# Kernel optimization log

Measured on AMD Instinct MI355X. Metric: run time of the kernel, lower is better.

The kernel has to match this reference:

```python
import jax, jax.numpy as jnp
import numpy as np

NUM_NODES = 17
NUM_REL = 8  # 4 edge types, doubled with reverse edges
IN_DIM = HID_DIM = OUT_DIM = 2048


def _build_graph():
    # Hardcoded brain graph from _build_brain_graph()
    # signals 0-5, emotions 6-11, cognitions 12-16
    src = np.array([0,0,1,1,2,2,3,3,4,4,5,5,          # signal->emotion (type 0)
                    6,6,7,7,8,8,8,9,9,10,11,11,       # emotion->cognition (type 1)
                    6,9,7,10,8,11,6,8,7,8,            # emotion<->emotion (type 2)
                    0,1,2])                            # signal->cognition (type 3)
    dst = np.array([7,10,6,9,9,7,10,7,6,9,9,6,
                    15,12,14,13,12,13,16,16,12,14,16,12,
                    9,6,10,7,11,8,8,6,8,7,
                    12,12,13])
    typ = np.array([0]*12 + [1]*12 + [2]*10 + [3]*3)
    # edge_index = cat([E, E.flip(0)]); edge_type = cat([t, t + 4])
    ei = np.stack([np.concatenate([src, dst]), np.concatenate([dst, src])])
    et = np.concatenate([typ, typ + 4])
    return jnp.asarray(ei, jnp.int32), jnp.asarray(et, jnp.int32)


def setup_inputs() -> dict:
    key = jax.random.key(0)
    ks = jax.random.split(key, 6)
    s = 0.02  # init scale
    edge_index, edge_type = _build_graph()
    return {
        'node_emb': jax.random.normal(ks[0], (NUM_NODES, IN_DIM), jnp.float32),
        'signal_features': jax.random.normal(ks[1], (6, IN_DIM), jnp.float32),
        'W1': jax.random.normal(ks[2], (NUM_REL, IN_DIM, HID_DIM), jnp.float32) * s,
        'root1': jax.random.normal(ks[3], (IN_DIM, HID_DIM), jnp.float32) * s,
        'bias1': jnp.zeros((HID_DIM,), jnp.float32),
        'W2': jax.random.normal(ks[4], (NUM_REL, HID_DIM, OUT_DIM), jnp.float32) * s,
        'root2': jax.random.normal(ks[5], (HID_DIM, OUT_DIM), jnp.float32) * s,
        'bias2': jnp.zeros((OUT_DIM,), jnp.float32),
        'edge_index': edge_index,
        'edge_type': edge_type,
    }


def _rgcn(x, W, root, bias, src, dst, etype):
    """PyG-style RGCNConv: per-relation linear + per-relation mean aggregation + root + bias."""
    # Transform all 17 nodes by all relations at once: [R, N, H] (tiny activation, avoids
    # gathering a [E, d, h] weight tensor per edge).
    xW = jnp.einsum('nd,rdh->rnh', x, W)
    msg = xW[etype, src]                                  # [E, H]
    seg = etype * NUM_NODES + dst                         # segment per (relation, target)
    sums = jax.ops.segment_sum(msg, seg, num_segments=NUM_REL * NUM_NODES)
    cnt = jax.ops.segment_sum(jnp.ones((msg.shape[0],), x.dtype), seg,
                              num_segments=NUM_REL * NUM_NODES)
    mean = sums / jnp.maximum(cnt, 1.0)[:, None]          # per-relation mean aggr
    agg = mean.reshape(NUM_REL, NUM_NODES, -1).sum(0)     # sum over relations
    return agg + x @ root + bias


def reference(node_emb, signal_features, W1, root1, bias1, W2, root2, bias2,
              edge_index, edge_type):
    src, dst = edge_index[0], edge_index[1]
    # h = node_emb(arange(17)); h[:6] = signal_features
    h = node_emb.at[:signal_features.shape[0]].set(signal_features)
    h1 = jax.nn.relu(_rgcn(h, W1, root1, bias1, src, dst, edge_type))
    # dropout is identity in eval mode
    h2 = _rgcn(h1, W2, root2, bias2, src, dst, edge_type)
    return h2
```

## Files before the change

kernel.cpp:

```cpp
#include <hip/hip_runtime.h>
#include <hip/hip_bf16.h>

#define D 2048
#define NTASK 55
#define NAGG 38
#define CHUNK 64
#define NCH 32

__constant__ int c_grp[10] = {0, 4, 9, 15, 17, 23, 29, 35, 38, 55};

__constant__ int c_src[74] = {
    1,4,5,  0,2,3,  1,2,4,5,  0,3,
    6,8,9,11,  7,8,  7,10,  6,  8,9,11,
    9,8,  10,8,  11,6,7,  6,  7,  8,
    0,1,  2,
    7,10,  6,9,  9,7,  10,7,  6,9,  9,6,
    15,12,  14,13,  12,13,16,  16,12,  14,  16,12,
    9,8,  10,8,  11,6,7,  6,  7,  8,
    12, 12, 13
};
__constant__ int c_off[39] = {
    0,3,6,10,12, 16,18,20,21,24, 26,28,31,32,33, 34,36,
    37,39,41,43,45,47, 49,51,53,56,58,59, 61,63,65,68,69,70, 71,72,73,74
};

__constant__ int c_node_tasks[38] = {
    17,35,  18,36,  19,37,  20,  21,  22,
    0,9,23,29,  1,10,24,30,  11,25,31,  2,12,26,32,  3,13,27,33,  14,28,34,
    4,15,  5,16,  6,  7,  8
};
__constant__ int c_node_off[18] = {0,2,4,6,7,8,9,13,17,20,24,28,31,33,35,36,37,38};

__global__ __launch_bounds__(256) void prep_kernel(
        const float* __restrict__ emb, const float* __restrict__ sig,
        float* __restrict__ U, float* __restrict__ TO) {
    int t = blockIdx.x;
    int tid = threadIdx.x;
    if (t >= NAGG) {
        int v = t - NAGG;
        const float* h = (v < 6) ? sig + (size_t)v * D : emb + (size_t)v * D;
        for (int c = tid; c < D; c += 256) {
            U[(size_t)t * D + c] = h[c];
            TO[(size_t)t * D + c] = 0.f;
        }
    } else {
        int o0 = c_off[t], o1 = c_off[t + 1];
        float cnt = (float)(o1 - o0);
        for (int c = tid; c < D; c += 256) {
            float s = 0.f;
            for (int o = o0; o < o1; ++o) {
                int sn = c_src[o];
                const float* h = (sn < 6) ? sig + (size_t)sn * D : emb + (size_t)sn * D;
                s += h[c];
            }
            U[(size_t)t * D + c] = s / cnt;
            TO[(size_t)t * D + c] = 0.f;
        }
    }
}

template <int NG>
__device__ __forceinline__ void gemm_inner(
        const float* __restrict__ Wg, const float* su,
        float* __restrict__ TO, int tb, int d0, int col) {
    float4 acc[NG];
#pragma unroll
    for (int t = 0; t < NG; ++t) acc[t] = make_float4(0.f, 0.f, 0.f, 0.f);
#pragma unroll 4
    for (int dd = 0; dd < CHUNK; ++dd) {
        float4 w = *reinterpret_cast<const float4*>(Wg + (size_t)(d0 + dd) * D + col);
#pragma unroll
        for (int t = 0; t < NG; ++t) {
            float u = su[t * CHUNK + dd];
            acc[t].x = fmaf(u, w.x, acc[t].x);
            acc[t].y = fmaf(u, w.y, acc[t].y);
            acc[t].z = fmaf(u, w.z, acc[t].z);
            acc[t].w = fmaf(u, w.w, acc[t].w);
        }
    }
#pragma unroll
    for (int t = 0; t < NG; ++t) {
        float* p = TO + (size_t)(tb + t) * D + col;
        atomicAdd(p + 0, acc[t].x);
        atomicAdd(p + 1, acc[t].y);
        atomicAdd(p + 2, acc[t].z);
        atomicAdd(p + 3, acc[t].w);
    }
}

__global__ __launch_bounds__(256) void gemm_kernel(
        const float* __restrict__ U, const float* __restrict__ W,
        const float* __restrict__ root, float* __restrict__ TO) {
    int b = blockIdx.x;
    int g = b >> 6;
    int r = b & 63;
    int ct = r & 1;
    int ch = r >> 1;
    int d0 = ch * CHUNK;
    int col = ct * 1024 + threadIdx.x * 4;
    const float* Wg = (g < 8) ? W + (size_t)g * D * D : root;
    int tb = c_grp[g];
    int ng = c_grp[g + 1] - tb;

    __shared__ float su[17 * CHUNK];
    for (int i = threadIdx.x; i < ng * CHUNK; i += 256) {
        int t = i >> 6, dd = i & (CHUNK - 1);
        su[i] = U[(size_t)(tb + t) * D + d0 + dd];
    }
    __syncthreads();

    switch (ng) {
        case 2:  gemm_inner<2>(Wg, su, TO, tb, d0, col); break;
        case 3:  gemm_inner<3>(Wg, su, TO, tb, d0, col); break;
        case 4:  gemm_inner<4>(Wg, su, TO, tb, d0, col); break;
        case 5:  gemm_inner<5>(Wg, su, TO, tb, d0, col); break;
        case 6:  gemm_inner<6>(Wg, su, TO, tb, d0, col); break;
        default: gemm_inner<17>(Wg, su, TO, tb, d0, col); break;
    }
}

__global__ __launch_bounds__(256) void mid_kernel(
        const float* __restrict__ bias, float* __restrict__ U,
        float* __restrict__ TO) {
    int c = blockIdx.x * 256 + threadIdx.x;
    int tid = threadIdx.x;
    __shared__ float h1s[17 * 256];
#pragma unroll
    for (int v = 0; v < 17; ++v) {
        float s = bias[c] + TO[(size_t)(NAGG + v) * D + c];
        for (int o = c_node_off[v]; o < c_node_off[v + 1]; ++o)
            s += TO[(size_t)c_node_tasks[o] * D + c];
        s = fmaxf(s, 0.f);
        h1s[v * 256 + tid] = s;
    }
    for (int t = 0; t < NAGG; ++t) {
        int o0 = c_off[t], o1 = c_off[t + 1];
        float s = 0.f;
        for (int o = o0; o < o1; ++o) s += h1s[c_src[o] * 256 + tid];
        U[(size_t)t * D + c] = s / (float)(o1 - o0);
        TO[(size_t)t * D + c] = 0.f;
    }
#pragma unroll
    for (int v = 0; v < 17; ++v) {
        U[(size_t)(NAGG + v) * D + c] = h1s[v * 256 + tid];
        TO[(size_t)(NAGG + v) * D + c] = 0.f;
    }
}

__global__ __launch_bounds__(256) void final_kernel(
        const float* __restrict__ TO, const float* __restrict__ bias,
        float* __restrict__ out) {
    int c = blockIdx.x * 256 + threadIdx.x;
#pragma unroll
    for (int v = 0; v < 17; ++v) {
        float s = bias[c] + TO[(size_t)(NAGG + v) * D + c];
        for (int o = c_node_off[v]; o < c_node_off[v + 1]; ++o)
            s += TO[(size_t)c_node_tasks[o] * D + c];
        out[(size_t)v * D + c] = s;
    }
}

extern "C" void kernel_launch(void* const* d_in, const int* in_sizes, int n_in,
                              void* d_out, int out_size, void* d_ws, size_t ws_size,
                              hipStream_t stream) {
    const float* emb   = (const float*)d_in[0];
    const float* sig   = (const float*)d_in[1];
    const float* W1    = (const float*)d_in[2];
    const float* root1 = (const float*)d_in[3];
    const float* b1    = (const float*)d_in[4];
    const float* W2    = (const float*)d_in[5];
    const float* root2 = (const float*)d_in[6];
    const float* b2    = (const float*)d_in[7];
    float* out = (float*)d_out;

    float* U  = (float*)d_ws;
    float* TO = U + (size_t)NTASK * D;

    prep_kernel<<<NTASK, 256, 0, stream>>>(emb, sig, U, TO);
    gemm_kernel<<<9 * 2 * NCH, 256, 0, stream>>>(U, W1, root1, TO);
    mid_kernel<<<D / 256, 256, 0, stream>>>(b1, U, TO);
    gemm_kernel<<<9 * 2 * NCH, 256, 0, stream>>>(U, W2, root2, TO);
    final_kernel<<<D / 256, 256, 0, stream>>>(TO, b2, out);
}
```

Before: 449.5 us.

## Replace atomic split-K accumulation with partial buffers and double-buffered weight loads

The GEMM no longer reduces split-K chunks with float atomicAdds into a zeroed accumulator. Each chunk writes its partials to its own slice of a P buffer, and the reduction over 32 chunks moves into the mid and final kernels, which now run across more blocks. Weight loads in the GEMM inner loop are software-pipelined with two 8-row register buffers so memory latency overlaps the FMAs. This removes atomic contention and the zeroing writes, but adds extra partial-buffer traffic, more register pressure, and one more kernel launch.

```diff
diff --git a/kernel.cpp b/kernel.cpp
--- a/kernel.cpp
+++ b/kernel.cpp
@@ -33,19 +33,17 @@
 
 __global__ __launch_bounds__(256) void prep_kernel(
         const float* __restrict__ emb, const float* __restrict__ sig,
-        float* __restrict__ U, float* __restrict__ TO) {
+        float* __restrict__ U) {
     int t = blockIdx.x;
     int tid = threadIdx.x;
     if (t >= NAGG) {
         int v = t - NAGG;
         const float* h = (v < 6) ? sig + (size_t)v * D : emb + (size_t)v * D;
-        for (int c = tid; c < D; c += 256) {
+        for (int c = tid; c < D; c += 256)
             U[(size_t)t * D + c] = h[c];
-            TO[(size_t)t * D + c] = 0.f;
-        }
     } else {
         int o0 = c_off[t], o1 = c_off[t + 1];
-        float cnt = (float)(o1 - o0);
+        float inv = 1.f / (float)(o1 - o0);
         for (int c = tid; c < D; c += 256) {
             float s = 0.f;
             for (int o = o0; o < o1; ++o) {
@@ -53,44 +51,52 @@
                 const float* h = (sn < 6) ? sig + (size_t)sn * D : emb + (size_t)sn * D;
                 s += h[c];
             }
-            U[(size_t)t * D + c] = s / cnt;
-            TO[(size_t)t * D + c] = 0.f;
+            U[(size_t)t * D + c] = s * inv;
         }
     }
 }
+
+#define LOADB(buf, base_row)                                                    \
+    _Pragma("unroll") for (int i_ = 0; i_ < 8; ++i_)                            \
+        buf[i_] = *reinterpret_cast<const float4*>(Wbase + (size_t)((base_row) + i_) * D);
+
+#define FMAB(buf, base_row)                                                     \
+    _Pragma("unroll") for (int i_ = 0; i_ < 8; ++i_) {                          \
+        _Pragma("unroll") for (int t_ = 0; t_ < NG; ++t_) {                     \
+            float u_ = su[t_ * CHUNK + (base_row) + i_];                        \
+            acc[t_].x = fmaf(u_, buf[i_].x, acc[t_].x);                         \
+            acc[t_].y = fmaf(u_, buf[i_].y, acc[t_].y);                         \
+            acc[t_].z = fmaf(u_, buf[i_].z, acc[t_].z);                         \
+            acc[t_].w = fmaf(u_, buf[i_].w, acc[t_].w);                         \
+        }                                                                       \
+    }
 
 template <int NG>
 __device__ __forceinline__ void gemm_inner(
-        const float* __restrict__ Wg, const float* su,
-        float* __restrict__ TO, int tb, int d0, int col) {
+        const float* __restrict__ Wbase, const float* su,
+        float* __restrict__ Pout) {
     float4 acc[NG];
 #pragma unroll
     for (int t = 0; t < NG; ++t) acc[t] = make_float4(0.f, 0.f, 0.f, 0.f);
-#pragma unroll 4
-    for (int dd = 0; dd < CHUNK; ++dd) {
-        float4 w = *reinterpret_cast<const float4*>(Wg + (size_t)(d0 + dd) * D + col);
-#pragma unroll
-        for (int t = 0; t < NG; ++t) {
-            float u = su[t * CHUNK + dd];
-            acc[t].x = fmaf(u, w.x, acc[t].x);
-            acc[t].y = fmaf(u, w.y, acc[t].y);
-            acc[t].z = fmaf(u, w.z, acc[t].z);
-            acc[t].w = fmaf(u, w.w, acc[t].w);
-        }
-    }
-#pragma unroll
-    for (int t = 0; t < NG; ++t) {
-        float* p = TO + (size_t)(tb + t) * D + col;
-        atomicAdd(p + 0, acc[t].x);
-        atomicAdd(p + 1, acc[t].y);
-        atomicAdd(p + 2, acc[t].z);
-        atomicAdd(p + 3, acc[t].w);
-    }
+    float4 wa[8], wb[8];
+    LOADB(wa, 0)
+    LOADB(wb, 8)
+    FMAB(wa, 0)   LOADB(wa, 16)
+    FMAB(wb, 8)   LOADB(wb, 24)
+    FMAB(wa, 16)  LOADB(wa, 32)
+    FMAB(wb, 24)  LOADB(wb, 40)
+    FMAB(wa, 32)  LOADB(wa, 48)
+    FMAB(wb, 40)  LOADB(wb, 56)
+    FMAB(wa, 48)
+    FMAB(wb, 56)
+#pragma unroll
+    for (int t = 0; t < NG; ++t)
+        *reinterpret_cast<float4*>(Pout + (size_t)t * D) = acc[t];
 }
 
 __global__ __launch_bounds__(256) void gemm_kernel(
         const float* __restrict__ U, const float* __restrict__ W,
-        const float* __restrict__ root, float* __restrict__ TO) {
+        const float* __restrict__ root, float* __restrict__ P) {
     int b = blockIdx.x;
     int g = b >> 6;
     int r = b & 63;
@@ -109,55 +115,70 @@
     }
     __syncthreads();
 
+    const float* Wbase = Wg + (size_t)d0 * D + col;
+    float* Pout = P + ((size_t)ch * NTASK + tb) * D + col;
+
     switch (ng) {
-        case 2:  gemm_inner<2>(Wg, su, TO, tb, d0, col); break;
-        case 3:  gemm_inner<3>(Wg, su, TO, tb, d0, col); break;
-        case 4:  gemm_inner<4>(Wg, su, TO, tb, d0, col); break;
-        case 5:  gemm_inner<5>(Wg, su, TO, tb, d0, col); break;
-        case 6:  gemm_inner<6>(Wg, su, TO, tb, d0, col); break;
-        default: gemm_inner<17>(Wg, su, TO, tb, d0, col); break;
-    }
-}
-
-__global__ __launch_bounds__(256) void mid_kernel(
-        const float* __restrict__ bias, float* __restrict__ U,
-        float* __restrict__ TO) {
-    int c = blockIdx.x * 256 + threadIdx.x;
-    int tid = threadIdx.x;
-    __shared__ float h1s[17 * 256];
-#pragma unroll
-    for (int v = 0; v < 17; ++v) {
-        float s = bias[c] + TO[(size_t)(NAGG + v) * D + c];
-        for (int o = c_node_off[v]; o < c_node_off[v + 1]; ++o)
-            s += TO[(size_t)c_node_tasks[o] * D + c];
-        s = fmaxf(s, 0.f);
-        h1s[v * 256 + tid] = s;
-    }
-    for (int t = 0; t < NAGG; ++t) {
+        case 2:  gemm_inner<2>(Wbase, su, Pout); break;
+        case 3:  gemm_inner<3>(Wbase, su, Pout); break;
+        case 4:  gemm_inner<4>(Wbase, su, Pout); break;
+        case 5:  gemm_inner<5>(Wbase, su, Pout); break;
+        case 6:  gemm_inner<6>(Wbase, su, Pout); break;
+        default: gemm_inner<17>(Wbase, su, Pout); break;
+    }
+}
+
+__global__ __launch_bounds__(256) void mid1_kernel(
+        const float* __restrict__ P, const float* __restrict__ bias,
+        float* __restrict__ h1) {
+    int idx = blockIdx.x * 256 + threadIdx.x;
+    int v = idx >> 11, col = idx & (D - 1);
+    float s = bias[col];
+    for (int o = c_node_off[v]; o < c_node_off[v + 1]; ++o) {
+        const float* p = P + (size_t)c_node_tasks[o] * D + col;
+#pragma unroll
+        for (int ch = 0; ch < NCH; ++ch) s += p[(size_t)ch * NTASK * D];
+    }
+    {
+        const float* p = P + (size_t)(NAGG + v) * D + col;
+#pragma unroll
+        for (int ch = 0; ch < NCH; ++ch) s += p[(size_t)ch * NTASK * D];
+    }
+    h1[idx] = fmaxf(s, 0.f);
+}
+
+__global__ __launch_bounds__(256) void u2_kernel(
+        const float* __restrict__ h1, float* __restrict__ U) {
+    int idx = blockIdx.x * 256 + threadIdx.x;
+    int t = idx >> 11, col = idx & (D - 1);
+    if (t >= NAGG) {
+        U[idx] = h1[(size_t)(t - NAGG) * D + col];
+    } else {
         int o0 = c_off[t], o1 = c_off[t + 1];
         float s = 0.f;
-        for (int o = o0; o < o1; ++o) s += h1s[c_src[o] * 256 + tid];
-        U[(size_t)t * D + c] = s / (float)(o1 - o0);
-        TO[(size_t)t * D + c] = 0.f;
-    }
-#pragma unroll
-    for (int v = 0; v < 17; ++v) {
-        U[(size_t)(NAGG + v) * D + c] = h1s[v * 256 + tid];
-        TO[(size_t)(NAGG + v) * D + c] = 0.f;
-    }
-}
-
-__global__ __launch_bounds__(256) void final_kernel(
-        const float* __restrict__ TO, const float* __restrict__ bias,
+        for (int o = o0; o < o1; ++o)
+            s += h1[(size_t)c_src[o] * D + col];
+        U[idx] = s / (float)(o1 - o0);
+    }
+}
+
+__global__ __launch_bounds__(256) void fin_kernel(
+        const float* __restrict__ P, const float* __restrict__ bias,
         float* __restrict__ out) {
-    int c = blockIdx.x * 256 + threadIdx.x;
-#pragma unroll
-    for (int v = 0; v < 17; ++v) {
-        float s = bias[c] + TO[(size_t)(NAGG + v) * D + c];
-        for (int o = c_node_off[v]; o < c_node_off[v + 1]; ++o)
-            s += TO[(size_t)c_node_tasks[o] * D + c];
-        out[(size_t)v * D + c] = s;
-    }
+    int idx = blockIdx.x * 256 + threadIdx.x;
+    int v = idx >> 11, col = idx & (D - 1);
+    float s = bias[col];
+    for (int o = c_node_off[v]; o < c_node_off[v + 1]; ++o) {
+        const float* p = P + (size_t)c_node_tasks[o] * D + col;
+#pragma unroll
+        for (int ch = 0; ch < NCH; ++ch) s += p[(size_t)ch * NTASK * D];
+    }
+    {
+        const float* p = P + (size_t)(NAGG + v) * D + col;
+#pragma unroll
+        for (int ch = 0; ch < NCH; ++ch) s += p[(size_t)ch * NTASK * D];
+    }
+    out[idx] = s;
 }
 
 extern "C" void kernel_launch(void* const* d_in, const int* in_sizes, int n_in,
@@ -174,11 +195,13 @@
     float* out = (float*)d_out;
 
     float* U  = (float*)d_ws;
-    float* TO = U + (size_t)NTASK * D;
-
-    prep_kernel<<<NTASK, 256, 0, stream>>>(emb, sig, U, TO);
-    gemm_kernel<<<9 * 2 * NCH, 256, 0, stream>>>(U, W1, root1, TO);
-    mid_kernel<<<D / 256, 256, 0, stream>>>(b1, U, TO);
-    gemm_kernel<<<9 * 2 * NCH, 256, 0, stream>>>(U, W2, root2, TO);
-    final_kernel<<<D / 256, 256, 0, stream>>>(TO, b2, out);
-}
+    float* h1 = U + (size_t)NTASK * D;
+    float* P  = h1 + (size_t)17 * D;
+
+    prep_kernel<<<NTASK, 256, 0, stream>>>(emb, sig, U);
+    gemm_kernel<<<9 * 2 * NCH, 256, 0, stream>>>(U, W1, root1, P);
+    mid1_kernel<<<17 * D / 256, 256, 0, stream>>>(P, b1, h1);
+    u2_kernel<<<NTASK * D / 256, 256, 0, stream>>>(h1, U);
+    gemm_kernel<<<9 * 2 * NCH, 256, 0, stream>>>(U, W2, root2, P);
+    fin_kernel<<<17 * D / 256, 256, 0, stream>>>(P, b2, out);
+}
```

Result: faster. 362.7 us (-19.3%).
